# Kernel tuning notes

Measured on AMD Instinct MI355X. Metric: run time of the kernel, lower is better.

Reference implementation:

```python
import jax, jax.numpy as jnp
import numpy as np

B, D, H, C, P, HP = 65536, 256, 512, 10, 10, 128


def setup_inputs() -> dict:
    key = jax.random.key(0)
    ks = jax.random.split(key, 6)
    return {
        "x": jax.random.normal(ks[0], (B, D), jnp.float32),
        "Wt1": jax.random.normal(ks[1], (D, H), jnp.float32) * (1.0 / np.sqrt(D)),
        "bt1": jnp.zeros((H,), jnp.float32),
        "Wt2": jax.random.normal(ks[2], (H, C), jnp.float32) * (1.0 / np.sqrt(H)),
        "bt2": jnp.zeros((C,), jnp.float32),
        "Wp1": jax.random.normal(ks[3], (P, D, HP), jnp.float32) * (1.0 / np.sqrt(D)),
        "bp1": jnp.zeros((P, HP), jnp.float32),
        "Wp2": jax.random.normal(ks[4], (P, HP, C), jnp.float32) * (1.0 / np.sqrt(HP)),
        "bp2": jnp.zeros((P, C), jnp.float32),
        "repair_direction_dict": jax.random.randint(ks[5], (P, 2), 0, C, jnp.int32),
    }


def _get_bitmap(out, rdd):
    # torch.topk(out, 2): indices of the two largest logits per row
    _, idx = jax.lax.top_k(out, 2)                                  # [B, 2]
    # is_in[b, p] = all(idx[b] == rdd[p])  (exact top-2 pair match)
    is_in = jnp.all(idx[:, None, :] == rdd[None, :, :], axis=-1)     # [B, P]
    no_match = ~jnp.any(is_in, axis=-1)                              # [B]
    # fallback for unmatched rows: top-1 index equals rdd[:, 0]
    fallback = idx[:, :1] == rdd[None, :, 0]                         # [B, P]
    return jnp.where(no_match[:, None], fallback, is_in)             # bool [B, P]


def reference(x, Wt1, bt1, Wt2, bt2, Wp1, bp1, Wp2, bp2, repair_direction_dict):
    # target net forward: out = target_net(x)
    out = jnp.maximum(x @ Wt1 + bt1, 0.0) @ Wt2 + bt2                # [B, C]
    # bitmap computed under no_grad in the original -> stop_gradient
    bitmap = jax.lax.stop_gradient(
        _get_bitmap(out, repair_direction_dict)
    ).astype(out.dtype)                                              # [B, P]
    # each patch net runs on the FULL batch (as in the original), then the
    # bitmap gates the scatter-add combine: out[bits] += p_out[bits]
    h = jnp.maximum(jnp.einsum('bd,pdh->pbh', x, Wp1) + bp1[:, None, :], 0.0)  # [P, B, HP]
    p_out = jnp.einsum('pbh,phc->pbc', h, Wp2) + bp2[:, None, :]     # [P, B, C]
    return out + jnp.einsum('bp,pbc->bc', bitmap, p_out)             # [B, C]
```

## Files before the change

kernel.cpp:

```cpp
#include <hip/hip_runtime.h>

typedef unsigned int u32;
typedef unsigned short u16;
typedef _Float16 f16;
typedef __attribute__((ext_vector_type(8))) _Float16 f16x8;
typedef __attribute__((ext_vector_type(4))) float f32x4;

#define MARGIN 1e-2f
#define LSC 2048.0f
#define LSCI (1.0f/2048.0f)

__device__ __forceinline__ u16 f16b(float f) {
    return __builtin_bit_cast(u16, (f16)f);
}
__device__ __forceinline__ f32x4 MF(f16x8 a, f16x8 b, f32x4 c) {
    return __builtin_amdgcn_mfma_f32_16x16x32_f16(a, b, c, 0, 0, 0);
}
__device__ __forceinline__ uint4 pack8(const u16 v[8]) {
    uint4 pk;
    pk.x = (u32)v[0] | ((u32)v[1] << 16);
    pk.y = (u32)v[2] | ((u32)v[3] << 16);
    pk.z = (u32)v[4] | ((u32)v[5] << 16);
    pk.w = (u32)v[6] | ((u32)v[7] << 16);
    return pk;
}

__global__ __launch_bounds__(256) void conv_kernel(
    const float* __restrict__ Wt1, const float* __restrict__ Wp1,
    const float* __restrict__ Wt2, const float* __restrict__ Wp2,
    u16* __restrict__ wt1f, u16* __restrict__ wt1g, u16* __restrict__ wp1f,
    u16* __restrict__ wt2f, u16* __restrict__ wt2g, u16* __restrict__ wp2f,
    u32* __restrict__ gcnt)
{
    __shared__ float tile[64][68];
    const int t = threadIdx.x;
    const int b = blockIdx.x;

    if (b == 112) {
        if (t == 0) gcnt[0] = 0;
        for (int cc = t; cc < 1024; cc += 256) {
            int kk = cc >> 6, l = cc & 63, ln = l & 15, quad = l >> 4;
            u16 vh[8], vl[8];
            #pragma unroll
            for (int j = 0; j < 8; ++j) {
                int k = kk * 32 + quad * 8 + j;
                float f = (ln < 10) ? Wt2[k * 10 + ln] : 0.f;
                f16 h = (f16)f;
                vh[j] = __builtin_bit_cast(u16, h);
                vl[j] = f16b(LSC * (f - (float)h));
            }
            *(uint4*)(wt2f + kk * 512 + l * 8) = pack8(vh);
            *(uint4*)(wt2g + kk * 512 + l * 8) = pack8(vl);
        }
        for (int cc = t; cc < 2560; cc += 256) {
            int p = cc >> 8, rem = cc & 255, kk = rem >> 6, l = rem & 63;
            int ln = l & 15, quad = (l >> 4) & 3;
            u16 v[8];
            #pragma unroll
            for (int j = 0; j < 8; ++j) {
                int k = kk * 32 + quad * 8 + j;
                v[j] = f16b(ln < 10 ? Wp2[p * 1280 + k * 10 + ln] : 0.f);
            }
            *(uint4*)(wp2f + p * 2048 + kk * 512 + l * 8) = pack8(v);
        }
        return;
    }

    const float* src; int src_ld;
    u16 *dsth, *dstl; int nf0, kk0;
    if (b < 32) {
        int kt = b & 3, nt = b >> 2;
        src = Wt1 + (size_t)(kt * 64) * 512 + nt * 64; src_ld = 512;
        dsth = wt1f; dstl = wt1g; nf0 = nt * 4; kk0 = kt * 2;
    } else {
        int j = b - 32, p = j >> 3, r = j & 7;
        int kt = r & 3, nt = r >> 2;
        src = Wp1 + (size_t)p * 32768 + (size_t)(kt * 64) * 128 + nt * 64; src_ld = 128;
        dsth = wp1f + p * 32768; dstl = nullptr; nf0 = nt * 4; kk0 = kt * 2;
    }
    {
        const int kr = t >> 2, c0 = (t & 3) * 16;
        #pragma unroll
        for (int u = 0; u < 4; ++u) {
            float4 v = *(const float4*)(src + (size_t)kr * src_ld + c0 + u * 4);
            tile[kr][c0 + u*4 + 0] = v.x;
            tile[kr][c0 + u*4 + 1] = v.y;
            tile[kr][c0 + u*4 + 2] = v.z;
            tile[kr][c0 + u*4 + 3] = v.w;
        }
    }
    __syncthreads();
    #pragma unroll
    for (int s = 0; s < 2; ++s) {
        int cc = t + 256 * s;
        int l = cc & 63, fp = cc >> 6, nfl = fp >> 1, kkl = fp & 1;
        int ln = l & 15, quad = (l >> 4) & 3;
        int nloc = nfl * 16 + ln, kloc = kkl * 32 + quad * 8;
        u16 vh[8], vl[8];
        #pragma unroll
        for (int j = 0; j < 8; ++j) {
            float f = tile[kloc + j][nloc];
            f16 h = (f16)f;
            vh[j] = __builtin_bit_cast(u16, h);
            vl[j] = f16b(LSC * (f - (float)h));
        }
        size_t off = (size_t)((nf0 + nfl) * 8 + (kk0 + kkl)) * 512 + l * 8;
        *(uint4*)(dsth + off) = pack8(vh);
        if (dstl) *(uint4*)(dstl + off) = pack8(vl);
    }
}

__global__ __launch_bounds__(512, 4) void netsum_kernel(
    const float* __restrict__ x, const float* __restrict__ bt1,
    const float* __restrict__ bt2,
    const float* __restrict__ bp1, const float* __restrict__ bp2,
    const int* __restrict__ rdd,
    const u16* __restrict__ wt1f, const u16* __restrict__ wp1f,
    const u16* __restrict__ wt2f, const u16* __restrict__ wp2f,
    float* __restrict__ out, u32* __restrict__ gcnt, u32* __restrict__ glist)
{
    __shared__ u16 xf[64][264];
    __shared__ u16 scratch[17408];
    __shared__ float lg[64][10];
    __shared__ float oacc[64][10];
    __shared__ u32 plist[10][64];
    __shared__ u32 pcnt[10];
    __shared__ int rdds[20];
    __shared__ u32 wq[40];
    __shared__ u32 nwork;

    const int t = threadIdx.x;
    const int lane = t & 63;
    const int w = t >> 6;
    const int ln = lane & 15;
    const int quad = lane >> 4;
    const int row0 = blockIdx.x * 64;

    if (t < 10) pcnt[t] = 0;
    if (t < 20) rdds[t] = rdd[t];
    if (t == 0) nwork = 0;
    for (int i = t; i < 640; i += 512) ((float*)oacc)[i] = 0.f;

    #pragma unroll
    for (int i = 0; i < 8; ++i) {
        int f = t + 512 * i;
        int r = f >> 6, c4 = f & 63;
        float4 v = *(const float4*)(x + (size_t)(row0 + r) * 256 + c4 * 4);
        u16 q0 = f16b(v.x), q1 = f16b(v.y), q2 = f16b(v.z), q3 = f16b(v.w);
        uint2 pw = { (u32)q0 | ((u32)q1 << 16), (u32)q2 | ((u32)q3 << 16) };
        *(uint2*)&xf[r][c4 * 4] = pw;
    }
    __syncthreads();

    f32x4 acc2 = (f32x4){0.f, 0.f, 0.f, 0.f};
    u16* hq = scratch;
    for (int q = 0; q < 4; ++q) {
        f32x4 acc[4];
        #pragma unroll
        for (int m = 0; m < 4; ++m) acc[m] = (f32x4){0.f,0.f,0.f,0.f};
        const u16* bb = wt1f + (size_t)((q * 8 + w) * 8) * 512 + (size_t)lane * 8;
        f16x8 wc = *(const f16x8*)bb;
        #pragma unroll
        for (int kk = 0; kk < 8; ++kk) {
            f16x8 wn = wc;
            if (kk < 7) wn = *(const f16x8*)(bb + (kk + 1) * 512);
            #pragma unroll
            for (int m = 0; m < 4; ++m) {
                f16x8 a = *(const f16x8*)(&xf[m * 16 + ln][kk * 32 + quad * 8]);
                acc[m] = MF(a, wc, acc[m]);
            }
            wc = wn;
        }
        {
            const int nloc = w * 16 + ln;
            const float bias = bt1[q * 128 + nloc];
            #pragma unroll
            for (int m = 0; m < 4; ++m)
                #pragma unroll
                for (int r = 0; r < 4; ++r) {
                    float hv = acc[m][r] + bias; hv = hv > 0.f ? hv : 0.f;
                    hq[(m * 16 + quad * 4 + r) * 136 + nloc] = f16b(hv);
                }
        }
        __syncthreads();
        if (w < 4) {
            #pragma unroll
            for (int kk2 = 0; kk2 < 4; ++kk2) {
                f16x8 ha = *(const f16x8*)(&hq[(w * 16 + ln) * 136 + kk2 * 32 + quad * 8]);
                f16x8 wb = *(const f16x8*)(wt2f + (q * 4 + kk2) * 512 + lane * 8);
                acc2 = MF(ha, wb, acc2);
            }
        }
        __syncthreads();
    }
    if (w < 4 && ln < 10) {
        #pragma unroll
        for (int r = 0; r < 4; ++r)
            lg[w * 16 + quad * 4 + r][ln] = acc2[r] + bt2[ln];
    }
    __syncthreads();

    if (t < 64) {
        float l[10];
        #pragma unroll
        for (int c = 0; c < 10; ++c) l[c] = lg[t][c];
        float b0 = -1e30f; int i0 = 0;
        #pragma unroll
        for (int c = 0; c < 10; ++c) if (l[c] > b0) { b0 = l[c]; i0 = c; }
        float b1 = -1e30f; int i1 = 0;
        #pragma unroll
        for (int c = 0; c < 10; ++c) { if (c == i0) continue; if (l[c] > b1) { b1 = l[c]; i1 = c; } }
        float b2v = -1e30f;
        #pragma unroll
        for (int c = 0; c < 10; ++c) { if (c == i0 || c == i1) continue; if (l[c] > b2v) b2v = l[c]; }
        if (b0 - b1 < MARGIN || b1 - b2v < MARGIN) {
            u32 idx = atomicAdd(gcnt, 1u);
            glist[idx] = (u32)(row0 + t);
        }
        u32 exact = 0, fb = 0;
        #pragma unroll
        for (int p = 0; p < 10; ++p) {
            int a = rdds[2 * p], bq = rdds[2 * p + 1];
            if (i0 == a && i1 == bq) exact |= 1u << p;
            if (i0 == a)             fb    |= 1u << p;
        }
        u32 bits = exact ? exact : fb;
        while (bits) {
            int p = __ffs(bits) - 1;
            bits &= bits - 1;
            u32 idx = atomicAdd(&pcnt[p], 1u);
            plist[p][idx] = (u32)t;
        }
    }
    __syncthreads();
    if (t < 10) {
        int L = (int)pcnt[t];
        for (int base = 0; base < L; base += 16) {
            u32 e = atomicAdd(&nwork, 1u);
            wq[e] = ((u32)t << 8) | (u32)base;
        }
    }
    __syncthreads();

    {
        const u32 nw = nwork;
        for (u32 ii = w; ii < nw; ii += 8) {
            const u32 item = wq[ii];
            const int p = (int)(item >> 8), mbase = (int)(item & 255);
            const int Lp = (int)pcnt[p];
            const int mi = mbase + ln;
            const int arow = (mi < Lp) ? (int)plist[p][mi] : (int)plist[p][0];
            const u16* xr = &xf[arow][0];
            const u16* wb = wp1f + (size_t)p * 32768 + (size_t)lane * 8;
            u16* hp = &scratch[w * 2176];
            #pragma unroll
            for (int g = 0; g < 2; ++g) {
                f32x4 acc4[4];
                #pragma unroll
                for (int i2 = 0; i2 < 4; ++i2) acc4[i2] = (f32x4){0.f,0.f,0.f,0.f};
                f16x8 wc4[4];
                #pragma unroll
                for (int i2 = 0; i2 < 4; ++i2)
                    wc4[i2] = *(const f16x8*)(wb + ((g * 4 + i2) * 8 + 0) * 512);
                #pragma unroll
                for (int kk = 0; kk < 8; ++kk) {
                    f16x8 wn4[4];
                    #pragma unroll
                    for (int i2 = 0; i2 < 4; ++i2) {
                        wn4[i2] = wc4[i2];
                        if (kk < 7)
                            wn4[i2] = *(const f16x8*)(wb + ((g * 4 + i2) * 8 + kk + 1) * 512);
                    }
                    f16x8 a = *(const f16x8*)(xr + kk * 32 + quad * 8);
                    #pragma unroll
                    for (int i2 = 0; i2 < 4; ++i2) acc4[i2] = MF(a, wc4[i2], acc4[i2]);
                    #pragma unroll
                    for (int i2 = 0; i2 < 4; ++i2) wc4[i2] = wn4[i2];
                }
                #pragma unroll
                for (int i2 = 0; i2 < 4; ++i2) {
                    const int i2g = g * 4 + i2;
                    float bias = bp1[p * 128 + i2g * 16 + ln];
                    #pragma unroll
                    for (int r = 0; r < 4; ++r) {
                        float hv = acc4[i2][r] + bias; hv = hv > 0.f ? hv : 0.f;
                        hp[(quad * 4 + r) * 136 + i2g * 16 + ln] = f16b(hv);
                    }
                }
            }
            f32x4 po = (f32x4){0.f,0.f,0.f,0.f};
            #pragma unroll
            for (int kk = 0; kk < 4; ++kk) {
                f16x8 ha = *(const f16x8*)(&hp[ln * 136 + kk * 32 + quad * 8]);
                f16x8 wb2 = *(const f16x8*)(wp2f + p * 2048 + kk * 512 + lane * 8);
                po = MF(ha, wb2, po);
            }
            if (ln < 10) {
                float b2 = bp2[p * 10 + ln];
                #pragma unroll
                for (int r = 0; r < 4; ++r) {
                    int mi2 = mbase + quad * 4 + r;
                    if (mi2 < Lp)
                        atomicAdd(&oacc[plist[p][mi2]][ln], po[r] + b2);
                }
            }
        }
    }
    __syncthreads();

    for (int i = t; i < 640; i += 512)
        out[(size_t)row0 * 10 + i] = ((float*)lg)[i] + ((float*)oacc)[i];
}

__global__ __launch_bounds__(512, 1) void fix_kernel(
    const float* __restrict__ x, const float* __restrict__ bt1,
    const float* __restrict__ bt2,
    const float* __restrict__ bp1, const float* __restrict__ bp2,
    const int* __restrict__ rdd,
    const u16* __restrict__ wt1f, const u16* __restrict__ wt1g,
    const u16* __restrict__ wt2f, const u16* __restrict__ wt2g,
    const u16* __restrict__ wp1f, const u16* __restrict__ wp2f,
    const u32* __restrict__ gcnt, const u32* __restrict__ glist,
    float* __restrict__ out)
{
    __shared__ u16 xfh[64][264];
    __shared__ u16 xfl[64][264];
    __shared__ u16 hb2[2][16896];
    __shared__ float lg[64][10];
    __shared__ float oacc[64][10];
    __shared__ u32 rows[64];
    __shared__ u32 plist[10][64];
    __shared__ u32 pcnt[10];
    __shared__ int rdds[20];
    __shared__ u32 wq[40];
    __shared__ u32 nwork;

    const int t = threadIdx.x;
    const int lane = t & 63;
    const int w = t >> 6;
    const int ln = lane & 15;
    const int quad = lane >> 4;
    const u32 cnt = gcnt[0];
    if (t < 20) rdds[t] = rdd[t];

    for (u32 base = blockIdx.x * 64; base < cnt; base += gridDim.x * 64) {
        __syncthreads();
        const int R = (int)min(64u, cnt - base);
        if (t < 64) rows[t] = glist[base + (t < R ? t : 0)];
        if (t < 10) pcnt[t] = 0;
        if (t == 0) nwork = 0;
        for (int i = t; i < 640; i += 512) ((float*)oacc)[i] = 0.f;
        __syncthreads();

        #pragma unroll
        for (int i = 0; i < 8; ++i) {
            int f = t + 512 * i;
            int r = f >> 6, c4 = f & 63;
            float4 v = *(const float4*)(x + (size_t)rows[r] * 256 + c4 * 4);
            f16 h0 = (f16)v.x, h1 = (f16)v.y, h2 = (f16)v.z, h3 = (f16)v.w;
            u16 q0 = __builtin_bit_cast(u16, h0), q1 = __builtin_bit_cast(u16, h1);
            u16 q2 = __builtin_bit_cast(u16, h2), q3 = __builtin_bit_cast(u16, h3);
            u16 l0 = f16b(LSC * (v.x - (float)h0)), l1 = f16b(LSC * (v.y - (float)h1));
            u16 l2 = f16b(LSC * (v.z - (float)h2)), l3 = f16b(LSC * (v.w - (float)h3));
            uint2 hw = { (u32)q0 | ((u32)q1 << 16), (u32)q2 | ((u32)q3 << 16) };
            uint2 lw = { (u32)l0 | ((u32)l1 << 16), (u32)l2 | ((u32)l3 << 16) };
            *(uint2*)&xfh[r][c4 * 4] = hw;
            *(uint2*)&xfl[r][c4 * 4] = lw;
        }
        __syncthreads();

        f32x4 acc2h = (f32x4){0.f,0.f,0.f,0.f};
        f32x4 acc2s = (f32x4){0.f,0.f,0.f,0.f};
        for (int hl = 0; hl < 2; ++hl) {
            f32x4 accH[4][2], accS[4][2];
            #pragma unroll
            for (int m = 0; m < 4; ++m)
                #pragma unroll
                for (int i2 = 0; i2 < 2; ++i2) {
                    accH[m][i2] = (f32x4){0.f,0.f,0.f,0.f};
                    accS[m][i2] = (f32x4){0.f,0.f,0.f,0.f};
                }
            const size_t boff = (size_t)(hl * 16 + w * 2) * 4096 + (size_t)lane * 8;
            const u16* bbh = wt1f + boff;
            const u16* bbl = wt1g + boff;
            #pragma unroll
            for (int kk = 0; kk < 8; ++kk) {
                f16x8 bh0 = *(const f16x8*)(bbh + kk * 512);
                f16x8 bh1 = *(const f16x8*)(bbh + 4096 + kk * 512);
                f16x8 bl0 = *(const f16x8*)(bbl + kk * 512);
                f16x8 bl1 = *(const f16x8*)(bbl + 4096 + kk * 512);
                #pragma unroll
                for (int m = 0; m < 4; ++m) {
                    f16x8 ah = *(const f16x8*)(&xfh[m * 16 + ln][kk * 32 + quad * 8]);
                    f16x8 al = *(const f16x8*)(&xfl[m * 16 + ln][kk * 32 + quad * 8]);
                    accH[m][0] = MF(ah, bh0, accH[m][0]);
                    accS[m][0] = MF(ah, bl0, accS[m][0]);
                    accS[m][0] = MF(al, bh0, accS[m][0]);
                    accH[m][1] = MF(ah, bh1, accH[m][1]);
                    accS[m][1] = MF(ah, bl1, accS[m][1]);
                    accS[m][1] = MF(al, bh1, accS[m][1]);
                }
            }
            #pragma unroll
            for (int m = 0; m < 4; ++m)
                #pragma unroll
                for (int i2 = 0; i2 < 2; ++i2) {
                    int nloc = w * 32 + i2 * 16 + ln;
                    float bias = bt1[hl * 256 + nloc];
                    #pragma unroll
                    for (int r = 0; r < 4; ++r) {
                        float hv = accH[m][i2][r] + accS[m][i2][r] * LSCI + bias;
                        hv = hv > 0.f ? hv : 0.f;
                        f16 hh = (f16)hv;
                        int idx = (m * 16 + quad * 4 + r) * 264 + nloc;
                        hb2[0][idx] = __builtin_bit_cast(u16, hh);
                        hb2[1][idx] = f16b(LSC * (hv - (float)hh));
                    }
                }
            __syncthreads();
            if (w < 4) {
                #pragma unroll
                for (int kk = 0; kk < 8; ++kk) {
                    int hidx = (w * 16 + ln) * 264 + kk * 32 + quad * 8;
                    f16x8 hah = *(const f16x8*)(&hb2[0][hidx]);
                    f16x8 hal = *(const f16x8*)(&hb2[1][hidx]);
                    f16x8 wbh = *(const f16x8*)(wt2f + (hl * 8 + kk) * 512 + lane * 8);
                    f16x8 wbl = *(const f16x8*)(wt2g + (hl * 8 + kk) * 512 + lane * 8);
                    acc2h = MF(hah, wbh, acc2h);
                    acc2s = MF(hah, wbl, acc2s);
                    acc2s = MF(hal, wbh, acc2s);
                }
            }
            __syncthreads();
        }
        if (w < 4 && ln < 10) {
            #pragma unroll
            for (int r = 0; r < 4; ++r)
                lg[w * 16 + quad * 4 + r][ln] = acc2h[r] + acc2s[r] * LSCI + bt2[ln];
        }
        __syncthreads();

        if (t < R) {
            float l[10];
            #pragma unroll
            for (int c = 0; c < 10; ++c) l[c] = lg[t][c];
            float b0 = -1e30f; int i0 = 0;
            #pragma unroll
            for (int c = 0; c < 10; ++c) if (l[c] > b0) { b0 = l[c]; i0 = c; }
            float b1 = -1e30f; int i1 = 0;
            #pragma unroll
            for (int c = 0; c < 10; ++c) { if (c == i0) continue; if (l[c] > b1) { b1 = l[c]; i1 = c; } }
            u32 exact = 0, fb = 0;
            #pragma unroll
            for (int p = 0; p < 10; ++p) {
                int a = rdds[2 * p], bq = rdds[2 * p + 1];
                if (i0 == a && i1 == bq) exact |= 1u << p;
                if (i0 == a)             fb    |= 1u << p;
            }
            u32 bits = exact ? exact : fb;
            while (bits) {
                int p = __ffs(bits) - 1;
                bits &= bits - 1;
                u32 idx = atomicAdd(&pcnt[p], 1u);
                plist[p][idx] = (u32)t;
            }
        }
        __syncthreads();
        if (t < 10) {
            int L = (int)pcnt[t];
            for (int b2 = 0; b2 < L; b2 += 16) {
                u32 e = atomicAdd(&nwork, 1u);
                wq[e] = ((u32)t << 8) | (u32)b2;
            }
        }
        __syncthreads();

        {
            const u32 nw = nwork;
            u16* hbuf = &hb2[0][0];
            for (u32 ii = w; ii < nw; ii += 8) {
                const u32 item = wq[ii];
                const int p = (int)(item >> 8), mbase = (int)(item & 255);
                const int Lp = (int)pcnt[p];
                const int mi = mbase + ln;
                const int arow = (mi < Lp) ? (int)plist[p][mi] : (int)plist[p][0];
                const u16* xr = &xfh[arow][0];
                const u16* wb = wp1f + (size_t)p * 32768 + (size_t)lane * 8;
                u16* hp = &hbuf[w * 2176];
                #pragma unroll
                for (int g = 0; g < 2; ++g) {
                    f32x4 acc4[4];
                    #pragma unroll
                    for (int i2 = 0; i2 < 4; ++i2) acc4[i2] = (f32x4){0.f,0.f,0.f,0.f};
                    f16x8 wc4[4];
                    #pragma unroll
                    for (int i2 = 0; i2 < 4; ++i2)
                        wc4[i2] = *(const f16x8*)(wb + ((g * 4 + i2) * 8 + 0) * 512);
                    #pragma unroll
                    for (int kk = 0; kk < 8; ++kk) {
                        f16x8 wn4[4];
                        #pragma unroll
                        for (int i2 = 0; i2 < 4; ++i2) {
                            wn4[i2] = wc4[i2];
                            if (kk < 7)
                                wn4[i2] = *(const f16x8*)(wb + ((g * 4 + i2) * 8 + kk + 1) * 512);
                        }
                        f16x8 a = *(const f16x8*)(xr + kk * 32 + quad * 8);
                        #pragma unroll
                        for (int i2 = 0; i2 < 4; ++i2) acc4[i2] = MF(a, wc4[i2], acc4[i2]);
                        #pragma unroll
                        for (int i2 = 0; i2 < 4; ++i2) wc4[i2] = wn4[i2];
                    }
                    #pragma unroll
                    for (int i2 = 0; i2 < 4; ++i2) {
                        const int i2g = g * 4 + i2;
                        float bias = bp1[p * 128 + i2g * 16 + ln];
                        #pragma unroll
                        for (int r = 0; r < 4; ++r) {
                            float hv = acc4[i2][r] + bias; hv = hv > 0.f ? hv : 0.f;
                            hp[(quad * 4 + r) * 136 + i2g * 16 + ln] = f16b(hv);
                        }
                    }
                }
                f32x4 po = (f32x4){0.f,0.f,0.f,0.f};
                #pragma unroll
                for (int kk = 0; kk < 4; ++kk) {
                    f16x8 ha = *(const f16x8*)(&hp[ln * 136 + kk * 32 + quad * 8]);
                    f16x8 wb2 = *(const f16x8*)(wp2f + p * 2048 + kk * 512 + lane * 8);
                    po = MF(ha, wb2, po);
                }
                if (ln < 10) {
                    float b2 = bp2[p * 10 + ln];
                    #pragma unroll
                    for (int r = 0; r < 4; ++r) {
                        int mi2 = mbase + quad * 4 + r;
                        if (mi2 < Lp)
                            atomicAdd(&oacc[plist[p][mi2]][ln], po[r] + b2);
                    }
                }
            }
        }
        __syncthreads();

        for (int i = t; i < R * 10; i += 512) {
            int r = i / 10, c = i % 10;
            out[(size_t)rows[r] * 10 + c] = lg[r][c] + oacc[r][c];
        }
    }
}

extern "C" void kernel_launch(void* const* d_in, const int* in_sizes, int n_in,
                              void* d_out, int out_size, void* d_ws, size_t ws_size,
                              hipStream_t stream) {
    const float* x   = (const float*)d_in[0];
    const float* Wt1 = (const float*)d_in[1];
    const float* bt1 = (const float*)d_in[2];
    const float* Wt2 = (const float*)d_in[3];
    const float* bt2 = (const float*)d_in[4];
    const float* Wp1 = (const float*)d_in[5];
    const float* bp1 = (const float*)d_in[6];
    const float* Wp2 = (const float*)d_in[7];
    const float* bp2 = (const float*)d_in[8];
    const int* rdd = (const int*)d_in[9];
    float* out = (float*)d_out;

    u16* wt1f = (u16*)d_ws;
    u16* wt1g = wt1f + 131072;
    u16* wp1f = wt1g + 131072;
    u16* wt2f = wp1f + 327680;
    u16* wt2g = wt2f + 8192;
    u16* wp2f = wt2g + 8192;
    u32* gcnt  = (u32*)(wp2f + 20480);
    u32* glist = gcnt + 16;

    hipLaunchKernelGGL(conv_kernel, dim3(113), dim3(256), 0, stream,
                       Wt1, Wp1, Wt2, Wp2, wt1f, wt1g, wp1f, wt2f, wt2g, wp2f, gcnt);
    hipLaunchKernelGGL(netsum_kernel, dim3(1024), dim3(512), 0, stream,
                       x, bt1, bt2, bp1, bp2, rdd,
                       wt1f, wp1f, wt2f, wp2f, out, gcnt, glist);
    hipLaunchKernelGGL(fix_kernel, dim3(256), dim3(512), 0, stream,
                       x, bt1, bt2, bp1, bp2, rdd,
                       wt1f, wt1g, wt2f, wt2g, wp1f, wp2f,
                       gcnt, glist, out);
}
```

Before: 198.5 us.

## Restructure target-net layer-1 tiling with register-resident x fragments and prefetched weights

The netsum target-net first layer is retiled so each wave owns one 16-row M group and half of the N columns. It keeps all eight x A-fragments in registers and software-pipelines the Wt1 B-fragment loads across N blocks and quarters. Hidden activations are stored transposed into a larger scratch buffer, and the second-layer Wt2 fragments are prefetched one quarter ahead. Launch bounds drop from 4 to 2 waves per SIMD to make room for the extra registers. In fix_kernel the layer-1 and layer-2 k-loops are manually double-buffered so weight loads overlap the MFMAs, at the cost of lower occupancy and strided LDS reads in l2afrag.

```diff
diff --git a/kernel.cpp b/kernel.cpp
--- a/kernel.cpp
+++ b/kernel.cpp
@@ -23,6 +23,12 @@
     pk.z = (u32)v[4] | ((u32)v[5] << 16);
     pk.w = (u32)v[6] | ((u32)v[7] << 16);
     return pk;
+}
+__device__ __forceinline__ f16x8 l2afrag(const u16* s, int kf, int quad, int row) {
+    union { u16 q[8]; f16x8 v; } u;
+    #pragma unroll
+    for (int j = 0; j < 8; ++j) u.q[j] = s[(kf * 32 + quad * 8 + j) * 72 + row];
+    return u.v;
 }
 
 __global__ __launch_bounds__(256) void conv_kernel(
@@ -110,7 +116,54 @@
     }
 }
 
-__global__ __launch_bounds__(512, 4) void netsum_kernel(
+#define LDQ(Q,J) (*(const f16x8*)(wt1f + (size_t)((Q)*64 + h2*32 + (J)) * 512 + lane*8))
+#define LDT(Q,K2) (*(const f16x8*)(wt2f + (size_t)((Q)*4+(K2))*512 + lane*8))
+
+#define HSTORE(Q,NFL) { \
+    const int colL = (h2*4+(NFL))*16 + ln; \
+    const float bias = bt1[(Q)*128 + colL]; \
+    ushort4 hv_; \
+    { float h_=acc[0]+bias; h_=h_>0.f?h_:0.f; hv_.x=f16b(h_); } \
+    { float h_=acc[1]+bias; h_=h_>0.f?h_:0.f; hv_.y=f16b(h_); } \
+    { float h_=acc[2]+bias; h_=h_>0.f?h_:0.f; hv_.z=f16b(h_); } \
+    { float h_=acc[3]+bias; h_=h_>0.f?h_:0.f; hv_.w=f16b(h_); } \
+    *(ushort4*)(scratch + colL*72 + mg*16 + quad*4) = hv_; }
+
+#define NFB_STD(Q,NFL) { f32x4 acc={0.f,0.f,0.f,0.f}; \
+    acc=MF(a0,bA,acc); bA=LDQ(Q,(NFL)*8+4); \
+    acc=MF(a1,bB,acc); bB=LDQ(Q,(NFL)*8+5); \
+    acc=MF(a2,bC,acc); bC=LDQ(Q,(NFL)*8+6); \
+    acc=MF(a3,bD,acc); bD=LDQ(Q,(NFL)*8+7); \
+    acc=MF(a4,bA,acc); bA=LDQ(Q,(NFL)*8+8); \
+    acc=MF(a5,bB,acc); bB=LDQ(Q,(NFL)*8+9); \
+    acc=MF(a6,bC,acc); bC=LDQ(Q,(NFL)*8+10); \
+    acc=MF(a7,bD,acc); bD=LDQ(Q,(NFL)*8+11); \
+    HSTORE(Q,NFL) }
+
+#define NFB_LAST(Q,QN) { f32x4 acc={0.f,0.f,0.f,0.f}; \
+    acc=MF(a0,bA,acc); bA=LDQ(Q,28); \
+    acc=MF(a1,bB,acc); bB=LDQ(Q,29); \
+    acc=MF(a2,bC,acc); bC=LDQ(Q,30); \
+    acc=MF(a3,bD,acc); bD=LDQ(Q,31); \
+    acc=MF(a4,bA,acc); bA=LDQ(QN,0); \
+    acc=MF(a5,bB,acc); bB=LDQ(QN,1); \
+    acc=MF(a6,bC,acc); bC=LDQ(QN,2); \
+    acc=MF(a7,bD,acc); bD=LDQ(QN,3); \
+    HSTORE(Q,3) }
+
+#define QUARTER9(Q,QN,LASTQ) \
+    NFB_STD(Q,0) NFB_STD(Q,1) NFB_STD(Q,2) NFB_LAST(Q,QN) \
+    __syncthreads(); \
+    if (w < 4) { \
+        f16x8 A0_=l2afrag(scratch,0,quad,w*16+ln), A1_=l2afrag(scratch,1,quad,w*16+ln); \
+        f16x8 A2_=l2afrag(scratch,2,quad,w*16+ln), A3_=l2afrag(scratch,3,quad,w*16+ln); \
+        acc2=MF(A0_,t0,acc2); acc2=MF(A1_,t1,acc2); \
+        acc2=MF(A2_,t2,acc2); acc2=MF(A3_,t3,acc2); \
+        if (!(LASTQ)) { t0=LDT((Q)+1,0); t1=LDT((Q)+1,1); t2=LDT((Q)+1,2); t3=LDT((Q)+1,3); } \
+    } \
+    __syncthreads();
+
+__global__ __launch_bounds__(512, 2) void netsum_kernel(
     const float* __restrict__ x, const float* __restrict__ bt1,
     const float* __restrict__ bt2,
     const float* __restrict__ bp1, const float* __restrict__ bp2,
@@ -120,7 +173,7 @@
     float* __restrict__ out, u32* __restrict__ gcnt, u32* __restrict__ glist)
 {
     __shared__ u16 xf[64][264];
-    __shared__ u16 scratch[17408];
+    __shared__ u16 scratch[17920];
     __shared__ float lg[64][10];
     __shared__ float oacc[64][10];
     __shared__ u32 plist[10][64];
@@ -134,6 +187,8 @@
     const int w = t >> 6;
     const int ln = lane & 15;
     const int quad = lane >> 4;
+    const int mg = w & 3;
+    const int h2 = w >> 2;
     const int row0 = blockIdx.x * 64;
 
     if (t < 10) pcnt[t] = 0;
@@ -150,49 +205,25 @@
         uint2 pw = { (u32)q0 | ((u32)q1 << 16), (u32)q2 | ((u32)q3 << 16) };
         *(uint2*)&xf[r][c4 * 4] = pw;
     }
+    f16x8 bA = LDQ(0,0), bB = LDQ(0,1), bC = LDQ(0,2), bD = LDQ(0,3);
+    f16x8 t0 = {}, t1 = {}, t2 = {}, t3 = {};
+    if (w < 4) { t0 = LDT(0,0); t1 = LDT(0,1); t2 = LDT(0,2); t3 = LDT(0,3); }
     __syncthreads();
 
+    f16x8 a0 = *(const f16x8*)(&xf[mg*16+ln][0*32 + quad*8]);
+    f16x8 a1 = *(const f16x8*)(&xf[mg*16+ln][1*32 + quad*8]);
+    f16x8 a2 = *(const f16x8*)(&xf[mg*16+ln][2*32 + quad*8]);
+    f16x8 a3 = *(const f16x8*)(&xf[mg*16+ln][3*32 + quad*8]);
+    f16x8 a4 = *(const f16x8*)(&xf[mg*16+ln][4*32 + quad*8]);
+    f16x8 a5 = *(const f16x8*)(&xf[mg*16+ln][5*32 + quad*8]);
+    f16x8 a6 = *(const f16x8*)(&xf[mg*16+ln][6*32 + quad*8]);
+    f16x8 a7 = *(const f16x8*)(&xf[mg*16+ln][7*32 + quad*8]);
+
     f32x4 acc2 = (f32x4){0.f, 0.f, 0.f, 0.f};
-    u16* hq = scratch;
-    for (int q = 0; q < 4; ++q) {
-        f32x4 acc[4];
-        #pragma unroll
-        for (int m = 0; m < 4; ++m) acc[m] = (f32x4){0.f,0.f,0.f,0.f};
-        const u16* bb = wt1f + (size_t)((q * 8 + w) * 8) * 512 + (size_t)lane * 8;
-        f16x8 wc = *(const f16x8*)bb;
-        #pragma unroll
-        for (int kk = 0; kk < 8; ++kk) {
-            f16x8 wn = wc;
-            if (kk < 7) wn = *(const f16x8*)(bb + (kk + 1) * 512);
-            #pragma unroll
-            for (int m = 0; m < 4; ++m) {
-                f16x8 a = *(const f16x8*)(&xf[m * 16 + ln][kk * 32 + quad * 8]);
-                acc[m] = MF(a, wc, acc[m]);
-            }
-            wc = wn;
-        }
-        {
-            const int nloc = w * 16 + ln;
-            const float bias = bt1[q * 128 + nloc];
-            #pragma unroll
-            for (int m = 0; m < 4; ++m)
-                #pragma unroll
-                for (int r = 0; r < 4; ++r) {
-                    float hv = acc[m][r] + bias; hv = hv > 0.f ? hv : 0.f;
-                    hq[(m * 16 + quad * 4 + r) * 136 + nloc] = f16b(hv);
-                }
-        }
-        __syncthreads();
-        if (w < 4) {
-            #pragma unroll
-            for (int kk2 = 0; kk2 < 4; ++kk2) {
-                f16x8 ha = *(const f16x8*)(&hq[(w * 16 + ln) * 136 + kk2 * 32 + quad * 8]);
-                f16x8 wb = *(const f16x8*)(wt2f + (q * 4 + kk2) * 512 + lane * 8);
-                acc2 = MF(ha, wb, acc2);
-            }
-        }
-        __syncthreads();
-    }
+    QUARTER9(0,1,0)
+    QUARTER9(1,2,0)
+    QUARTER9(2,3,0)
+    QUARTER9(3,3,1)
     if (w < 4 && ln < 10) {
         #pragma unroll
         for (int r = 0; r < 4; ++r)
@@ -204,16 +235,16 @@
         float l[10];
         #pragma unroll
         for (int c = 0; c < 10; ++c) l[c] = lg[t][c];
-        float b0 = -1e30f; int i0 = 0;
-        #pragma unroll
-        for (int c = 0; c < 10; ++c) if (l[c] > b0) { b0 = l[c]; i0 = c; }
-        float b1 = -1e30f; int i1 = 0;
-        #pragma unroll
-        for (int c = 0; c < 10; ++c) { if (c == i0) continue; if (l[c] > b1) { b1 = l[c]; i1 = c; } }
+        float b0v = -1e30f; int i0 = 0;
+        #pragma unroll
+        for (int c = 0; c < 10; ++c) if (l[c] > b0v) { b0v = l[c]; i0 = c; }
+        float b1v = -1e30f; int i1 = 0;
+        #pragma unroll
+        for (int c = 0; c < 10; ++c) { if (c == i0) continue; if (l[c] > b1v) { b1v = l[c]; i1 = c; } }
         float b2v = -1e30f;
         #pragma unroll
         for (int c = 0; c < 10; ++c) { if (c == i0 || c == i1) continue; if (l[c] > b2v) b2v = l[c]; }
-        if (b0 - b1 < MARGIN || b1 - b2v < MARGIN) {
+        if (b0v - b1v < MARGIN || b1v - b2v < MARGIN) {
             u32 idx = atomicAdd(gcnt, 1u);
             glist[idx] = (u32)(row0 + t);
         }
@@ -311,6 +342,23 @@
     for (int i = t; i < 640; i += 512)
         out[(size_t)row0 * 10 + i] = ((float*)lg)[i] + ((float*)oacc)[i];
 }
+
+#define FLD(S,KK) \
+    S##h0 = *(const f16x8*)(bbh + (KK)*512); \
+    S##h1 = *(const f16x8*)(bbh + 4096 + (KK)*512); \
+    S##l0 = *(const f16x8*)(bbl + (KK)*512); \
+    S##l1 = *(const f16x8*)(bbl + 4096 + (KK)*512);
+#define FCP(S,KK) { _Pragma("unroll") for (int m_=0;m_<4;++m_){ \
+    f16x8 ah_=*(const f16x8*)(&xfh[m_*16+ln][(KK)*32+quad*8]); \
+    f16x8 al_=*(const f16x8*)(&xfl[m_*16+ln][(KK)*32+quad*8]); \
+    accH[m_][0]=MF(ah_,S##h0,accH[m_][0]); accS[m_][0]=MF(ah_,S##l0,accS[m_][0]); accS[m_][0]=MF(al_,S##h0,accS[m_][0]); \
+    accH[m_][1]=MF(ah_,S##h1,accH[m_][1]); accS[m_][1]=MF(ah_,S##l1,accS[m_][1]); accS[m_][1]=MF(al_,S##h1,accS[m_][1]); } }
+#define F2L(WH, WL, KK) \
+    WH = *(const f16x8*)(wt2f + (hl*8+(KK))*512 + lane*8); \
+    WL = *(const f16x8*)(wt2g + (hl*8+(KK))*512 + lane*8);
+#define F2C(WH, WL, KK) { int hidx_=(w*16+ln)*264 + (KK)*32 + quad*8; \
+    f16x8 hah_=*(const f16x8*)(&hb2[0][hidx_]); f16x8 hal_=*(const f16x8*)(&hb2[1][hidx_]); \
+    acc2h=MF(hah_,WH,acc2h); acc2s=MF(hah_,WL,acc2s); acc2s=MF(hal_,WH,acc2s); }
 
 __global__ __launch_bounds__(512, 1) void fix_kernel(
     const float* __restrict__ x, const float* __restrict__ bt1,
@@ -383,24 +431,16 @@
             const size_t boff = (size_t)(hl * 16 + w * 2) * 4096 + (size_t)lane * 8;
             const u16* bbh = wt1f + boff;
             const u16* bbl = wt1g + boff;
-            #pragma unroll
-            for (int kk = 0; kk < 8; ++kk) {
-                f16x8 bh0 = *(const f16x8*)(bbh + kk * 512);
-                f16x8 bh1 = *(const f16x8*)(bbh + 4096 + kk * 512);
-                f16x8 bl0 = *(const f16x8*)(bbl + kk * 512);
-                f16x8 bl1 = *(const f16x8*)(bbl + 4096 + kk * 512);
-                #pragma unroll
-                for (int m = 0; m < 4; ++m) {
-                    f16x8 ah = *(const f16x8*)(&xfh[m * 16 + ln][kk * 32 + quad * 8]);
-                    f16x8 al = *(const f16x8*)(&xfl[m * 16 + ln][kk * 32 + quad * 8]);
-                    accH[m][0] = MF(ah, bh0, accH[m][0]);
-                    accS[m][0] = MF(ah, bl0, accS[m][0]);
-                    accS[m][0] = MF(al, bh0, accS[m][0]);
-                    accH[m][1] = MF(ah, bh1, accH[m][1]);
-                    accS[m][1] = MF(ah, bl1, accS[m][1]);
-                    accS[m][1] = MF(al, bh1, accS[m][1]);
-                }
-            }
+            f16x8 ch0, ch1, cl0, cl1, nh0, nh1, nl0, nl1;
+            FLD(c,0);
+            FLD(n,1); FCP(c,0);
+            FLD(c,2); FCP(n,1);
+            FLD(n,3); FCP(c,2);
+            FLD(c,4); FCP(n,3);
+            FLD(n,5); FCP(c,4);
+            FLD(c,6); FCP(n,5);
+            FLD(n,7); FCP(c,6);
+            FCP(n,7);
             #pragma unroll
             for (int m = 0; m < 4; ++m)
                 #pragma unroll
@@ -419,17 +459,16 @@
                 }
             __syncthreads();
             if (w < 4) {
-                #pragma unroll
-                for (int kk = 0; kk < 8; ++kk) {
-                    int hidx = (w * 16 + ln) * 264 + kk * 32 + quad * 8;
-                    f16x8 hah = *(const f16x8*)(&hb2[0][hidx]);
-                    f16x8 hal = *(const f16x8*)(&hb2[1][hidx]);
-                    f16x8 wbh = *(const f16x8*)(wt2f + (hl * 8 + kk) * 512 + lane * 8);
-                    f16x8 wbl = *(const f16x8*)(wt2g + (hl * 8 + kk) * 512 + lane * 8);
-                    acc2h = MF(hah, wbh, acc2h);
-                    acc2s = MF(hah, wbl, acc2s);
-                    acc2s = MF(hal, wbh, acc2s);
-                }
+                f16x8 whc, wlc, whn, wln;
+                F2L(whc, wlc, 0);
+                F2L(whn, wln, 1); F2C(whc, wlc, 0);
+                F2L(whc, wlc, 2); F2C(whn, wln, 1);
+                F2L(whn, wln, 3); F2C(whc, wlc, 2);
+                F2L(whc, wlc, 4); F2C(whn, wln, 3);
+                F2L(whn, wln, 5); F2C(whc, wlc, 4);
+                F2L(whc, wlc, 6); F2C(whn, wln, 5);
+                F2L(whn, wln, 7); F2C(whc, wlc, 6);
+                F2C(whn, wln, 7);
             }
             __syncthreads();
         }
@@ -444,12 +483,12 @@
             float l[10];
             #pragma unroll
             for (int c = 0; c < 10; ++c) l[c] = lg[t][c];
-            float b0 = -1e30f; int i0 = 0;
-            #pragma unroll
-            for (int c = 0; c < 10; ++c) if (l[c] > b0) { b0 = l[c]; i0 = c; }
-            float b1 = -1e30f; int i1 = 0;
-            #pragma unroll
-            for (int c = 0; c < 10; ++c) { if (c == i0) continue; if (l[c] > b1) { b1 = l[c]; i1 = c; } }
+            float b0v = -1e30f; int i0 = 0;
+            #pragma unroll
+            for (int c = 0; c < 10; ++c) if (l[c] > b0v) { b0v = l[c]; i0 = c; }
+            float b1v = -1e30f; int i1 = 0;
+            #pragma unroll
+            for (int c = 0; c < 10; ++c) { if (c == i0) continue; if (l[c] > b1v) { b1v = l[c]; i1 = c; } }
             u32 exact = 0, fb = 0;
             #pragma unroll
             for (int p = 0; p < 10; ++p) {
@@ -468,16 +507,16 @@
         __syncthreads();
         if (t < 10) {
             int L = (int)pcnt[t];
-            for (int b2 = 0; b2 < L; b2 += 16) {
+            for (int b2i = 0; b2i < L; b2i += 16) {
                 u32 e = atomicAdd(&nwork, 1u);
-                wq[e] = ((u32)t << 8) | (u32)b2;
+                wq[e] = ((u32)t << 8) | (u32)b2i;
             }
         }
         __syncthreads();
 
         {
             const u32 nw = nwork;
-            u16* hbuf = &hb2[0][0];
+            u16* hbase = &hb2[0][0];
             for (u32 ii = w; ii < nw; ii += 8) {
                 const u32 item = wq[ii];
                 const int p = (int)(item >> 8), mbase = (int)(item & 255);
@@ -486,7 +525,7 @@
                 const int arow = (mi < Lp) ? (int)plist[p][mi] : (int)plist[p][0];
                 const u16* xr = &xfh[arow][0];
                 const u16* wb = wp1f + (size_t)p * 32768 + (size_t)lane * 8;
-                u16* hp = &hbuf[w * 2176];
+                u16* hp = hbase + w * 2176;
                 #pragma unroll
                 for (int g = 0; g < 2; ++g) {
                     f32x4 acc4[4];
```

New measurement: 209.3 us. 1.05x slower.

## Shrink fix_kernel tiles to 16 rows, split second GEMM across warps, raise occupancy

Applied to the files above, without the earlier changes.

Restructures the high-precision fix-up kernel to process 16 flagged rows per iteration instead of 64, cutting shared memory so two blocks can reside per CU, and launches 1024 blocks instead of 256. The first-layer GEMM becomes a single M-tile with software-pipelined double-buffered weight loads. The second-layer GEMM is split over K across four warps, with results combined through shared-memory atomics into bias-initialised logits. Patch work items become one per patch. This trades per-block weight reuse for more parallelism on the small set of near-tie rows, and adds more global weight traffic per row.

```diff
diff --git a/kernel.cpp b/kernel.cpp
--- a/kernel.cpp
+++ b/kernel.cpp
@@ -204,16 +204,16 @@
         float l[10];
         #pragma unroll
         for (int c = 0; c < 10; ++c) l[c] = lg[t][c];
-        float b0 = -1e30f; int i0 = 0;
-        #pragma unroll
-        for (int c = 0; c < 10; ++c) if (l[c] > b0) { b0 = l[c]; i0 = c; }
-        float b1 = -1e30f; int i1 = 0;
-        #pragma unroll
-        for (int c = 0; c < 10; ++c) { if (c == i0) continue; if (l[c] > b1) { b1 = l[c]; i1 = c; } }
+        float b0v = -1e30f; int i0 = 0;
+        #pragma unroll
+        for (int c = 0; c < 10; ++c) if (l[c] > b0v) { b0v = l[c]; i0 = c; }
+        float b1v = -1e30f; int i1 = 0;
+        #pragma unroll
+        for (int c = 0; c < 10; ++c) { if (c == i0) continue; if (l[c] > b1v) { b1v = l[c]; i1 = c; } }
         float b2v = -1e30f;
         #pragma unroll
         for (int c = 0; c < 10; ++c) { if (c == i0 || c == i1) continue; if (l[c] > b2v) b2v = l[c]; }
-        if (b0 - b1 < MARGIN || b1 - b2v < MARGIN) {
+        if (b0v - b1v < MARGIN || b1v - b2v < MARGIN) {
             u32 idx = atomicAdd(gcnt, 1u);
             glist[idx] = (u32)(row0 + t);
         }
@@ -312,7 +312,24 @@
         out[(size_t)row0 * 10 + i] = ((float*)lg)[i] + ((float*)oacc)[i];
 }
 
-__global__ __launch_bounds__(512, 1) void fix_kernel(
+#define FLD(S,KK) \
+    S##h0 = *(const f16x8*)(bbh + (KK)*512); \
+    S##h1 = *(const f16x8*)(bbh + 4096 + (KK)*512); \
+    S##l0 = *(const f16x8*)(bbl + (KK)*512); \
+    S##l1 = *(const f16x8*)(bbl + 4096 + (KK)*512);
+#define FCP(S,KK) { \
+    f16x8 ah_=*(const f16x8*)(&xfh[ln][(KK)*32+quad*8]); \
+    f16x8 al_=*(const f16x8*)(&xfl[ln][(KK)*32+quad*8]); \
+    accH0=MF(ah_,S##h0,accH0); accS0=MF(ah_,S##l0,accS0); accS0=MF(al_,S##h0,accS0); \
+    accH1=MF(ah_,S##h1,accH1); accS1=MF(ah_,S##l1,accS1); accS1=MF(al_,S##h1,accS1); }
+#define F2L(WH, WL, KK) \
+    WH = *(const f16x8*)(wt2f + (hl*8+(KK))*512 + lane*8); \
+    WL = *(const f16x8*)(wt2g + (hl*8+(KK))*512 + lane*8);
+#define F2C(WH, WL, KK) { int hidx_ = ln*264 + (KK)*32 + quad*8; \
+    f16x8 hah_=*(const f16x8*)(&hb2[0][hidx_]); f16x8 hal_=*(const f16x8*)(&hb2[1][hidx_]); \
+    acc2h=MF(hah_,WH,acc2h); acc2s=MF(hah_,WL,acc2s); acc2s=MF(hal_,WH,acc2s); }
+
+__global__ __launch_bounds__(512, 2) void fix_kernel(
     const float* __restrict__ x, const float* __restrict__ bt1,
     const float* __restrict__ bt2,
     const float* __restrict__ bp1, const float* __restrict__ bp2,
@@ -323,16 +340,17 @@
     const u32* __restrict__ gcnt, const u32* __restrict__ glist,
     float* __restrict__ out)
 {
-    __shared__ u16 xfh[64][264];
-    __shared__ u16 xfl[64][264];
-    __shared__ u16 hb2[2][16896];
-    __shared__ float lg[64][10];
-    __shared__ float oacc[64][10];
-    __shared__ u32 rows[64];
-    __shared__ u32 plist[10][64];
+    __shared__ u16 xfh[16][264];
+    __shared__ u16 xfl[16][264];
+    __shared__ u16 hb2[2][4224];
+    __shared__ u16 hpbuf[17408];
+    __shared__ float lgx[16][10];
+    __shared__ float oacc[16][10];
+    __shared__ u32 rows[16];
+    __shared__ u32 plist[10][16];
     __shared__ u32 pcnt[10];
     __shared__ int rdds[20];
-    __shared__ u32 wq[40];
+    __shared__ u32 wq[16];
     __shared__ u32 nwork;
 
     const int t = threadIdx.x;
@@ -343,17 +361,20 @@
     const u32 cnt = gcnt[0];
     if (t < 20) rdds[t] = rdd[t];
 
-    for (u32 base = blockIdx.x * 64; base < cnt; base += gridDim.x * 64) {
-        __syncthreads();
-        const int R = (int)min(64u, cnt - base);
-        if (t < 64) rows[t] = glist[base + (t < R ? t : 0)];
+    for (u32 base = blockIdx.x * 16; base < cnt; base += gridDim.x * 16) {
+        __syncthreads();
+        const int R = (int)min(16u, cnt - base);
+        if (t < 16) rows[t] = glist[base + (t < R ? t : 0)];
         if (t < 10) pcnt[t] = 0;
         if (t == 0) nwork = 0;
-        for (int i = t; i < 640; i += 512) ((float*)oacc)[i] = 0.f;
-        __syncthreads();
-
-        #pragma unroll
-        for (int i = 0; i < 8; ++i) {
+        if (t < 160) {
+            ((float*)lgx)[t] = bt2[t % 10];
+            ((float*)oacc)[t] = 0.f;
+        }
+        __syncthreads();
+
+        #pragma unroll
+        for (int i = 0; i < 2; ++i) {
             int f = t + 512 * i;
             int r = f >> 6, c4 = f & 63;
             float4 v = *(const float4*)(x + (size_t)rows[r] * 256 + c4 * 4);
@@ -372,84 +393,63 @@
         f32x4 acc2h = (f32x4){0.f,0.f,0.f,0.f};
         f32x4 acc2s = (f32x4){0.f,0.f,0.f,0.f};
         for (int hl = 0; hl < 2; ++hl) {
-            f32x4 accH[4][2], accS[4][2];
-            #pragma unroll
-            for (int m = 0; m < 4; ++m)
-                #pragma unroll
-                for (int i2 = 0; i2 < 2; ++i2) {
-                    accH[m][i2] = (f32x4){0.f,0.f,0.f,0.f};
-                    accS[m][i2] = (f32x4){0.f,0.f,0.f,0.f};
-                }
+            f32x4 accH0 = (f32x4){0.f,0.f,0.f,0.f}, accH1 = accH0;
+            f32x4 accS0 = accH0, accS1 = accH0;
             const size_t boff = (size_t)(hl * 16 + w * 2) * 4096 + (size_t)lane * 8;
             const u16* bbh = wt1f + boff;
             const u16* bbl = wt1g + boff;
-            #pragma unroll
-            for (int kk = 0; kk < 8; ++kk) {
-                f16x8 bh0 = *(const f16x8*)(bbh + kk * 512);
-                f16x8 bh1 = *(const f16x8*)(bbh + 4096 + kk * 512);
-                f16x8 bl0 = *(const f16x8*)(bbl + kk * 512);
-                f16x8 bl1 = *(const f16x8*)(bbl + 4096 + kk * 512);
-                #pragma unroll
-                for (int m = 0; m < 4; ++m) {
-                    f16x8 ah = *(const f16x8*)(&xfh[m * 16 + ln][kk * 32 + quad * 8]);
-                    f16x8 al = *(const f16x8*)(&xfl[m * 16 + ln][kk * 32 + quad * 8]);
-                    accH[m][0] = MF(ah, bh0, accH[m][0]);
-                    accS[m][0] = MF(ah, bl0, accS[m][0]);
-                    accS[m][0] = MF(al, bh0, accS[m][0]);
-                    accH[m][1] = MF(ah, bh1, accH[m][1]);
-                    accS[m][1] = MF(ah, bl1, accS[m][1]);
-                    accS[m][1] = MF(al, bh1, accS[m][1]);
-                }
-            }
-            #pragma unroll
-            for (int m = 0; m < 4; ++m)
-                #pragma unroll
-                for (int i2 = 0; i2 < 2; ++i2) {
-                    int nloc = w * 32 + i2 * 16 + ln;
-                    float bias = bt1[hl * 256 + nloc];
-                    #pragma unroll
-                    for (int r = 0; r < 4; ++r) {
-                        float hv = accH[m][i2][r] + accS[m][i2][r] * LSCI + bias;
-                        hv = hv > 0.f ? hv : 0.f;
-                        f16 hh = (f16)hv;
-                        int idx = (m * 16 + quad * 4 + r) * 264 + nloc;
-                        hb2[0][idx] = __builtin_bit_cast(u16, hh);
-                        hb2[1][idx] = f16b(LSC * (hv - (float)hh));
-                    }
-                }
+            f16x8 ch0, ch1, cl0, cl1, nh0, nh1, nl0, nl1;
+            FLD(c,0);
+            FLD(n,1); FCP(c,0);
+            FLD(c,2); FCP(n,1);
+            FLD(n,3); FCP(c,2);
+            FLD(c,4); FCP(n,3);
+            FLD(n,5); FCP(c,4);
+            FLD(c,6); FCP(n,5);
+            FLD(n,7); FCP(c,6);
+            FCP(n,7);
+            #pragma unroll
+            for (int i2 = 0; i2 < 2; ++i2) {
+                int nloc = w * 32 + i2 * 16 + ln;
+                float bias = bt1[hl * 256 + nloc];
+                #pragma unroll
+                for (int r = 0; r < 4; ++r) {
+                    float hv = (i2 == 0 ? accH0[r] + accS0[r] * LSCI
+                                        : accH1[r] + accS1[r] * LSCI) + bias;
+                    hv = hv > 0.f ? hv : 0.f;
+                    f16 hh = (f16)hv;
+                    int idx = (quad * 4 + r) * 264 + nloc;
+                    hb2[0][idx] = __builtin_bit_cast(u16, hh);
+                    hb2[1][idx] = f16b(LSC * (hv - (float)hh));
+                }
+            }
             __syncthreads();
             if (w < 4) {
-                #pragma unroll
-                for (int kk = 0; kk < 8; ++kk) {
-                    int hidx = (w * 16 + ln) * 264 + kk * 32 + quad * 8;
-                    f16x8 hah = *(const f16x8*)(&hb2[0][hidx]);
-                    f16x8 hal = *(const f16x8*)(&hb2[1][hidx]);
-                    f16x8 wbh = *(const f16x8*)(wt2f + (hl * 8 + kk) * 512 + lane * 8);
-                    f16x8 wbl = *(const f16x8*)(wt2g + (hl * 8 + kk) * 512 + lane * 8);
-                    acc2h = MF(hah, wbh, acc2h);
-                    acc2s = MF(hah, wbl, acc2s);
-                    acc2s = MF(hal, wbh, acc2s);
-                }
+                f16x8 whA, wlA, whB, wlB;
+                F2L(whA, wlA, w);
+                F2L(whB, wlB, w + 4);
+                F2C(whA, wlA, w);
+                F2C(whB, wlB, w + 4);
             }
             __syncthreads();
         }
         if (w < 4 && ln < 10) {
             #pragma unroll
             for (int r = 0; r < 4; ++r)
-                lg[w * 16 + quad * 4 + r][ln] = acc2h[r] + acc2s[r] * LSCI + bt2[ln];
+                atomicAdd(&lgx[quad * 4 + r][ln], acc2h[r] + acc2s[r] * LSCI);
         }
         __syncthreads();
 
         if (t < R) {
             float l[10];
             #pragma unroll
-            for (int c = 0; c < 10; ++c) l[c] = lg[t][c];
-            float b0 = -1e30f; int i0 = 0;
-            #pragma unroll
-            for (int c = 0; c < 10; ++c) if (l[c] > b0) { b0 = l[c]; i0 = c; }
-            float b1 = -1e30f; int i1 = 0;
-            #pragma unroll
-            for (int c = 0; c < 10; ++c) { if (c == i0) continue; if (l[c] > b1) { b1 = l[c]; i1 = c; } }
+            for (int c = 0; c < 10; ++c) l[c] = lgx[t][c];
+            float b0v = -1e30f; int i0 = 0;
+            #pragma unroll
+            for (int c = 0; c < 10; ++c) if (l[c] > b0v) { b0v = l[c]; i0 = c; }
+            float b1v = -1e30f; int i1 = 0;
+            #pragma unroll
+            for (int c = 0; c < 10; ++c) { if (c == i0) continue; if (l[c] > b1v) { b1v = l[c]; i1 = c; } }
             u32 exact = 0, fb = 0;
             #pragma unroll
             for (int p = 0; p < 10; ++p) {
@@ -466,27 +466,21 @@
             }
         }
         __syncthreads();
-        if (t < 10) {
-            int L = (int)pcnt[t];
-            for (int b2 = 0; b2 < L; b2 += 16) {
-                u32 e = atomicAdd(&nwork, 1u);
-                wq[e] = ((u32)t << 8) | (u32)b2;
-            }
+        if (t < 10 && pcnt[t] > 0) {
+            u32 e = atomicAdd(&nwork, 1u);
+            wq[e] = (u32)t;
         }
         __syncthreads();
 
         {
             const u32 nw = nwork;
-            u16* hbuf = &hb2[0][0];
             for (u32 ii = w; ii < nw; ii += 8) {
-                const u32 item = wq[ii];
-                const int p = (int)(item >> 8), mbase = (int)(item & 255);
+                const int p = (int)wq[ii];
                 const int Lp = (int)pcnt[p];
-                const int mi = mbase + ln;
-                const int arow = (mi < Lp) ? (int)plist[p][mi] : (int)plist[p][0];
+                const int arow = (ln < Lp) ? (int)plist[p][ln] : (int)plist[p][0];
                 const u16* xr = &xfh[arow][0];
                 const u16* wb = wp1f + (size_t)p * 32768 + (size_t)lane * 8;
-                u16* hp = &hbuf[w * 2176];
+                u16* hp = &hpbuf[w * 2176];
                 #pragma unroll
                 for (int g = 0; g < 2; ++g) {
                     f32x4 acc4[4];
@@ -533,7 +527,7 @@
                     float b2 = bp2[p * 10 + ln];
                     #pragma unroll
                     for (int r = 0; r < 4; ++r) {
-                        int mi2 = mbase + quad * 4 + r;
+                        int mi2 = quad * 4 + r;
                         if (mi2 < Lp)
                             atomicAdd(&oacc[plist[p][mi2]][ln], po[r] + b2);
                     }
@@ -542,9 +536,9 @@
         }
         __syncthreads();
 
-        for (int i = t; i < R * 10; i += 512) {
-            int r = i / 10, c = i % 10;
-            out[(size_t)rows[r] * 10 + c] = lg[r][c] + oacc[r][c];
+        if (t < R * 10) {
+            int r = t / 10, c = t % 10;
+            out[(size_t)rows[r] * 10 + c] = lgx[r][c] + oacc[r][c];
         }
     }
 }
@@ -578,7 +572,7 @@
     hipLaunchKernelGGL(netsum_kernel, dim3(1024), dim3(512), 0, stream,
                        x, bt1, bt2, bp1, bp2, rdd,
                        wt1f, wp1f, wt2f, wp2f, out, gcnt, glist);
-    hipLaunchKernelGGL(fix_kernel, dim3(256), dim3(512), 0, stream,
+    hipLaunchKernelGGL(fix_kernel, dim3(1024), dim3(512), 0, stream,
                        x, bt1, bt2, bp1, bp2, rdd,
                        wt1f, wt1g, wt2f, wt2g, wp1f, wp2f,
                        gcnt, glist, out);
```

After: 218.4 us. 10.0% more time.
